# Kernel tuning notes

Measured on AMD Instinct MI355X. Metric: run time of the kernel, lower is better.

## Reference

```python
import jax, jax.numpy as jnp
import numpy as np

DIM = 384
K = 7          # kernel_size
FINAL = 16     # final_size
DROP_P = 0.2


def setup_inputs() -> dict:
    key = jax.random.key(0)
    k1, k2, k3, k4, k5, k6 = jax.random.split(key, 6)
    hr_feats = jax.random.normal(k1, (8, DIM, 112, 112), jnp.float32)
    guidance = jnp.zeros((1,), jnp.float32)  # unused by forward
    dropout_u = jax.random.uniform(k2, (8, FINAL, FINAL, 1), jnp.float32)
    aw = jax.random.normal(k3, (DIM,), jnp.float32) / np.sqrt(DIM).astype(np.float32)
    ab = 0.01 * jax.random.normal(k4, (1,), jnp.float32)
    w = 1.0 + 0.01 * jax.random.normal(k5, (K, K), jnp.float32)
    b = 0.01 * jax.random.normal(k6, (K, K), jnp.float32)
    return {"hr_feats": hr_feats, "guidance": guidance, "dropout_u": dropout_u,
            "aw": aw, "ab": ab, "w": w, "b": b}


def _unfold_patches(x):
    # x: [b, c, h, w] -> [b, nH, nW, K*K, c], matching torch Unfold + reshape/permute
    bs, c, h, wd = x.shape
    stride = (h - K) // (FINAL - 1)
    nH = FINAL
    nW = FINAL * (wd // h)
    r = (jnp.arange(nH) * stride)[:, None] + jnp.arange(K)      # [nH, K]
    cc = (jnp.arange(nW) * stride)[:, None] + jnp.arange(K)     # [nW, K]
    # advanced indexing -> [b, c, nH, nW, K, K]
    patches = x[:, :, r[:, None, :, None], cc[None, :, None, :]]
    # (kh, kw) flattened row-major, channel last -> same ordering as torch Unfold
    return patches.transpose(0, 2, 3, 4, 5, 1).reshape(bs, nH, nW, K * K, c)


def reference(hr_feats, guidance, dropout_u, aw, ab, w, b):
    patches = _unfold_patches(hr_feats)                    # [b, H, W, P, C]
    # attention_net (eval-mode Dropout is identity): Linear(dim, 1)
    logits = jnp.einsum('bhwpc,c->bhwp', patches, aw) + ab[0]
    mask = (dropout_u > DROP_P).astype(logits.dtype)       # [b, H, W, 1]
    attn_logits = logits * mask * w.reshape(1, 1, 1, -1) + b.reshape(1, 1, 1, -1)
    attn = jax.nn.softmax(attn_logits, axis=-1)            # softmax over patches
    return jnp.einsum('bhwpc,bhwp->bchw', patches, attn)   # [b, C, H, W]
```

## Files before the change

kernel.cpp:

```cpp
#include <hip/hip_runtime.h>
#include <cmath>

#define DIM 384
#define IMG 112
#define IMG2 (IMG*IMG)
#define FINALN 16
#define PATCH 49
#define DROP_P 0.2f

#define SLABC 64
#define SLABF (SLABC*392)

__global__ __launch_bounds__(512) void kRow(const float* __restrict__ hr,
                                            const float* __restrict__ du,
                                            const float* __restrict__ aw,
                                            const float* __restrict__ ab,
                                            const float* __restrict__ wmat,
                                            const float* __restrict__ bmat,
                                            float* __restrict__ out) {
    __shared__ float slab[SLABF];
    __shared__ float s_aw[DIM];
    __shared__ float attn_s[8 * 50];

    int tid  = threadIdx.x;
    int id   = blockIdx.x;
    int nid  = (id & 7) * 32 + (id >> 3);
    int b  = nid >> 5;
    int h  = (nid >> 1) & 15;
    int wh = nid & 1;

    if (tid < DIM) s_aw[tid] = aw[tid];

    const float* base = hr + (size_t)b * DIM * IMG2 + (size_t)(7 * h) * IMG + 56 * wh;

    int c_sub = tid / 98;
    int q     = tid - c_sub * 98;
    int i1 = q / 14, cq1 = q - i1 * 14;
    __syncthreads();

    if (tid < 392) {
        const float* gp = base + (size_t)c_sub * IMG2 + i1 * IMG + 4 * cq1;
        float l0 = 0.f, l1 = 0.f, l2 = 0.f, l3 = 0.f;
        int awi = c_sub;
        #pragma unroll 8
        for (int it = 0; it < 96; ++it) {
            float4 v = *reinterpret_cast<const float4*>(gp);
            float av = s_aw[awi];
            l0 = fmaf(v.x, av, l0);
            l1 = fmaf(v.y, av, l1);
            l2 = fmaf(v.z, av, l2);
            l3 = fmaf(v.w, av, l3);
            gp += (size_t)4 * IMG2;
            awi += 4;
        }
        float4 st = make_float4(l0, l1, l2, l3);
        *reinterpret_cast<float4*>(&slab[c_sub * 400 + 4 * q]) = st;
    }
    __syncthreads();

    {
        int ww = tid >> 6, l = tid & 63;
        float al = -1e30f;
        if (l < PATCH) {
            int li = l / 7, lj = l - li * 7;
            int pos = li * 56 + 7 * ww + lj;
            float logit = slab[pos] + slab[400 + pos] + slab[800 + pos] + slab[1200 + pos];
            float duv  = du[(b << 8) + (h << 4) + (wh << 3) + ww];
            float mask = (duv > DROP_P) ? 1.0f : 0.0f;
            al = fmaf((logit + ab[0]) * mask, wmat[l], bmat[l]);
        }
        float m = al;
        #pragma unroll
        for (int d = 32; d >= 1; d >>= 1) m = fmaxf(m, __shfl_xor(m, d, 64));
        float e = (l < PATCH) ? __expf(al - m) : 0.f;
        float s = e;
        #pragma unroll
        for (int d = 32; d >= 1; d >>= 1) s += __shfl_xor(s, d, 64);
        if (l < PATCH) attn_s[ww * 50 + l] = e / s;
    }
    __syncthreads();

    int wloc = tid & 7;
    int cs   = tid >> 3;
    float attw[PATCH];
    #pragma unroll
    for (int p = 0; p < PATCH; ++p) attw[p] = attn_s[wloc * 50 + p];

    int goff[13], loff[13];
    #pragma unroll
    for (int k = 0; k < 13; ++k) {
        int idx = tid + 512 * k;
        int c = idx / 98, qq = idx - c * 98;
        int ii = qq / 14, cq = qq - ii * 14;
        goff[k] = c * IMG2 + ii * IMG + 4 * cq;
        loff[k] = idx * 4;
    }

    size_t ob = ((size_t)b * DIM + cs) * 256 + (h << 4) + (wh << 3) + wloc;

    for (int cc = 0; cc < 6; ++cc) {
        const float* cb = base + (size_t)(cc * SLABC) * IMG2;
        #pragma unroll
        for (int k = 0; k < 12; ++k)
            *reinterpret_cast<float4*>(&slab[loff[k]]) =
                *reinterpret_cast<const float4*>(cb + goff[k]);
        if (tid < 128)
            *reinterpret_cast<float4*>(&slab[loff[12]]) =
                *reinterpret_cast<const float4*>(cb + goff[12]);
        __syncthreads();

        float o = 0.f;
        const float* sr = &slab[cs * 392 + 7 * wloc];
        #pragma unroll
        for (int p = 0; p < PATCH; ++p) {
            const int pi = p / 7, pj = p - (p / 7) * 7;
            o = fmaf(sr[pi * 56 + pj], attw[p], o);
        }
        out[ob + (size_t)(cc * SLABC) * 256] = o;
        if (cc < 5) __syncthreads();
    }
}

extern "C" void kernel_launch(void* const* d_in, const int* in_sizes, int n_in,
                              void* d_out, int out_size, void* d_ws, size_t ws_size,
                              hipStream_t stream) {
    const float* hr   = (const float*)d_in[0];
    const float* du   = (const float*)d_in[2];
    const float* aw   = (const float*)d_in[3];
    const float* ab   = (const float*)d_in[4];
    const float* wmat = (const float*)d_in[5];
    const float* bmat = (const float*)d_in[6];
    float* out = (float*)d_out;

    kRow<<<256, 512, 0, stream>>>(hr, du, aw, ab, wmat, bmat, out);
}
```

Baseline: 242.1 us.

## Cache patch values as fp16 in registers to read input once

Instead of reading the feature slab from global memory a second time for the weighted sum, each thread keeps the values it loaded during the logit pass as half2 in a 192-entry register array. It then writes them into an fp16 shared slab per channel chunk. This aims to halve global traffic. The costs are heavy register pressure, with likely spilling under launch_bounds(512,2), and fp16 rounding of the output values.

```diff
diff --git a/kernel.cpp b/kernel.cpp
--- a/kernel.cpp
+++ b/kernel.cpp
@@ -1,4 +1,5 @@
 #include <hip/hip_runtime.h>
+#include <hip/hip_fp16.h>
 #include <cmath>
 
 #define DIM 384
@@ -8,53 +9,51 @@
 #define PATCH 49
 #define DROP_P 0.2f
 
-#define SLABC 64
-#define SLABF (SLABC*392)
-
-__global__ __launch_bounds__(512) void kRow(const float* __restrict__ hr,
-                                            const float* __restrict__ du,
-                                            const float* __restrict__ aw,
-                                            const float* __restrict__ ab,
-                                            const float* __restrict__ wmat,
-                                            const float* __restrict__ bmat,
-                                            float* __restrict__ out) {
-    __shared__ float slab[SLABF];
+__global__ __launch_bounds__(512, 2) void kOnePass(const float* __restrict__ hr,
+                                                   const float* __restrict__ du,
+                                                   const float* __restrict__ aw,
+                                                   const float* __restrict__ ab,
+                                                   const float* __restrict__ wmat,
+                                                   const float* __restrict__ bmat,
+                                                   float* __restrict__ out) {
+    __shared__ __half slabh[64 * 392];
     __shared__ float s_aw[DIM];
+    __shared__ float lacc[4 * 400];
     __shared__ float attn_s[8 * 50];
 
-    int tid  = threadIdx.x;
-    int id   = blockIdx.x;
-    int nid  = (id & 7) * 32 + (id >> 3);
+    int tid = threadIdx.x;
+    int id  = blockIdx.x;
+    int nid = (id & 7) * 32 + (id >> 3);
     int b  = nid >> 5;
     int h  = (nid >> 1) & 15;
     int wh = nid & 1;
 
     if (tid < DIM) s_aw[tid] = aw[tid];
+    __syncthreads();
 
     const float* base = hr + (size_t)b * DIM * IMG2 + (size_t)(7 * h) * IMG + 56 * wh;
 
     int c_sub = tid / 98;
     int q     = tid - c_sub * 98;
-    int i1 = q / 14, cq1 = q - i1 * 14;
-    __syncthreads();
+    int i1 = q / 14, cq = q - i1 * 14;
 
+    __half2 hv[192];
     if (tid < 392) {
-        const float* gp = base + (size_t)c_sub * IMG2 + i1 * IMG + 4 * cq1;
+        const float* gp = base + (size_t)c_sub * IMG2 + i1 * IMG + 4 * cq;
         float l0 = 0.f, l1 = 0.f, l2 = 0.f, l3 = 0.f;
-        int awi = c_sub;
-        #pragma unroll 8
-        for (int it = 0; it < 96; ++it) {
-            float4 v = *reinterpret_cast<const float4*>(gp);
-            float av = s_aw[awi];
+        #pragma unroll
+        for (int k = 0; k < 96; ++k) {
+            float4 v = *reinterpret_cast<const float4*>(gp + (size_t)(4 * k) * IMG2);
+            float av = s_aw[4 * k + c_sub];
             l0 = fmaf(v.x, av, l0);
             l1 = fmaf(v.y, av, l1);
             l2 = fmaf(v.z, av, l2);
             l3 = fmaf(v.w, av, l3);
-            gp += (size_t)4 * IMG2;
-            awi += 4;
+            hv[2 * k]     = __floats2half2_rn(v.x, v.y);
+            hv[2 * k + 1] = __floats2half2_rn(v.z, v.w);
         }
-        float4 st = make_float4(l0, l1, l2, l3);
-        *reinterpret_cast<float4*>(&slab[c_sub * 400 + 4 * q]) = st;
+        *reinterpret_cast<float4*>(&lacc[c_sub * 400 + 4 * q]) =
+            make_float4(l0, l1, l2, l3);
     }
     __syncthreads();
 
@@ -64,7 +63,7 @@
         if (l < PATCH) {
             int li = l / 7, lj = l - li * 7;
             int pos = li * 56 + 7 * ww + lj;
-            float logit = slab[pos] + slab[400 + pos] + slab[800 + pos] + slab[1200 + pos];
+            float logit = lacc[pos] + lacc[400 + pos] + lacc[800 + pos] + lacc[1200 + pos];
             float duv  = du[(b << 8) + (h << 4) + (wh << 3) + ww];
             float mask = (duv > DROP_P) ? 1.0f : 0.0f;
             al = fmaf((logit + ab[0]) * mask, wmat[l], bmat[l]);
@@ -82,42 +81,35 @@
 
     int wloc = tid & 7;
     int cs   = tid >> 3;
-    float attw[PATCH];
-    #pragma unroll
-    for (int p = 0; p < PATCH; ++p) attw[p] = attn_s[wloc * 50 + p];
-
-    int goff[13], loff[13];
-    #pragma unroll
-    for (int k = 0; k < 13; ++k) {
-        int idx = tid + 512 * k;
-        int c = idx / 98, qq = idx - c * 98;
-        int ii = qq / 14, cq = qq - ii * 14;
-        goff[k] = c * IMG2 + ii * IMG + 4 * cq;
-        loff[k] = idx * 4;
-    }
-
     size_t ob = ((size_t)b * DIM + cs) * 256 + (h << 4) + (wh << 3) + wloc;
 
+    float attw[PATCH];
+
     for (int cc = 0; cc < 6; ++cc) {
-        const float* cb = base + (size_t)(cc * SLABC) * IMG2;
-        #pragma unroll
-        for (int k = 0; k < 12; ++k)
-            *reinterpret_cast<float4*>(&slab[loff[k]]) =
-                *reinterpret_cast<const float4*>(cb + goff[k]);
-        if (tid < 128)
-            *reinterpret_cast<float4*>(&slab[loff[12]]) =
-                *reinterpret_cast<const float4*>(cb + goff[12]);
+        if (cc) __syncthreads();
+        if (tid < 392) {
+            #pragma unroll
+            for (int kk = 0; kk < 16; ++kk) {
+                int c_local = 4 * kk + c_sub;
+                *reinterpret_cast<uint2*>(&slabh[c_local * 392 + 4 * q]) =
+                    *reinterpret_cast<const uint2*>(&hv[2 * (16 * cc + kk)]);
+            }
+        }
         __syncthreads();
 
+        if (cc == 0) {
+            #pragma unroll
+            for (int p = 0; p < PATCH; ++p) attw[p] = attn_s[wloc * 50 + p];
+        }
+
         float o = 0.f;
-        const float* sr = &slab[cs * 392 + 7 * wloc];
+        const __half* sr = &slabh[cs * 392 + 7 * wloc];
         #pragma unroll
         for (int p = 0; p < PATCH; ++p) {
-            const int pi = p / 7, pj = p - (p / 7) * 7;
-            o = fmaf(sr[pi * 56 + pj], attw[p], o);
+            const int pi = p / 7, pj = p - pi * 7;
+            o = fmaf(__half2float(sr[pi * 56 + pj]), attw[p], o);
         }
-        out[ob + (size_t)(cc * SLABC) * 256] = o;
-        if (cc < 5) __syncthreads();
+        out[ob + (size_t)(cc * 64) * 256] = o;
     }
 }
 
@@ -132,5 +124,5 @@
     const float* bmat = (const float*)d_in[6];
     float* out = (float*)d_out;
 
-    kRow<<<256, 512, 0, stream>>>(hr, du, aw, ab, wmat, bmat, out);
+    kOnePass<<<256, 512, 0, stream>>>(hr, du, aw, ab, wmat, bmat, out);
 }
```

Result: no change. 241.8 us (-0.1%).
